# Kernel tuning notes

Hardware: AMD Instinct MI355X
Metric: run time of the kernel (lower is better)

The kernel has to match this reference:

```python
import jax, jax.numpy as jnp
import numpy as np

N = 128      # numNodes
F_IN = 128   # numFeatures
H = 64       # numHiddens
C = 40       # numClasses
K = 2        # numLayers (SGConv hops)
B = 4096     # batch
NTRIL = N * (N + 1) // 2


def setup_inputs() -> dict:
    key = jax.random.key(0)
    ks = jax.random.split(key, 6)
    x = jax.random.normal(ks[0], (B, N, F_IN), dtype=jnp.float32)
    edge_w = jax.random.uniform(ks[1], (NTRIL,), dtype=jnp.float32)  # learnable tril edge weights (positive init)
    lin_w = jax.random.normal(ks[2], (F_IN, H), dtype=jnp.float32) / np.float32(np.sqrt(F_IN))
    lin_b = jnp.zeros((H,), dtype=jnp.float32)
    conv_w = jax.random.normal(ks[3], (N,), dtype=jnp.float32) / np.float32(np.sqrt(N))  # Conv1d(N,1,1) weight
    conv_b = jnp.zeros((1,), dtype=jnp.float32)
    fc_w = jax.random.normal(ks[4], (H, C), dtype=jnp.float32) / np.float32(np.sqrt(H))
    fc_b = jnp.zeros((C,), dtype=jnp.float32)
    return {"x": x, "edge_w": edge_w, "lin_w": lin_w, "lin_b": lin_b,
            "conv_w": conv_w, "conv_b": conv_b, "fc_w": fc_w, "fc_b": fc_b}


def reference(x, edge_w, lin_w, lin_b, conv_w, conv_b, fc_w, fc_b):
    # Rebuild symmetric dense adjacency from tril-parameterized edge weights
    xs, ys = jnp.tril_indices(N)
    A = jnp.zeros((N, N), dtype=jnp.float32).at[xs, ys].set(edge_w)
    A = A + A.T - jnp.diag(jnp.diag(A))                 # symmetrize (keep diag once)
    A_hat = A + jnp.eye(N, dtype=jnp.float32)           # add_self_loops(fill_value=1)
    # SGConv symmetric normalization: D^-1/2 (A+I) D^-1/2
    deg = A_hat.sum(axis=1)
    dinv = jnp.where(deg > 0, deg ** -0.5, 0.0)
    A_norm = dinv[:, None] * A_hat * dinv[None, :]
    # K-hop propagation over node dim (memory-bound stream of [B,N,F])
    h = x
    for _ in range(K):
        h = jnp.einsum('ij,bjf->bif', A_norm, h)
    h = jax.nn.relu(h @ lin_w + lin_b)                  # SGConv linear + relu -> [B,N,H]
    pooled = jnp.einsum('bnh,n->bh', h, conv_w) + conv_b  # Conv1d(N->1, kernel=1) over nodes
    pooled = jax.nn.relu(pooled)
    return pooled @ fc_w + fc_b                         # [B, C]
```

## Files before the change

kernel.cpp:

```cpp
#include <hip/hip_runtime.h>
#include <math.h>

#define N     128
#define F_INN 128
#define HD    64
#define NC    40
#define BB    4096

#define CHUNK     16
#define XS_STRIDE 17
#define YS_STRIDE 68

__global__ void prep_anorm(const float* __restrict__ edge_w,
                           float* __restrict__ An_out) {
    __shared__ float Ah[N][N + 1];
    __shared__ float dinv[N];
    const int t  = threadIdx.x;
    const int i  = t >> 1;
    const int jh = (t & 1) * 64;
    for (int jj = 0; jj < 64; ++jj) {
        int j  = jh + jj;
        int hi = i >= j ? i : j;
        int lo = i >= j ? j : i;
        float a = edge_w[hi * (hi + 1) / 2 + lo];
        if (i == j) a += 1.0f;
        Ah[i][j] = a;
    }
    __syncthreads();
    if (t < N) {
        float s = 0.0f;
        for (int j = 0; j < N; ++j) s += Ah[t][j];
        dinv[t] = s > 0.0f ? 1.0f / sqrtf(s) : 0.0f;
    }
    __syncthreads();
    for (int jj = 0; jj < 64; ++jj) {
        int j = jh + jj;
        An_out[i * N + j] = dinv[i] * Ah[i][j] * dinv[j];
    }
}

__global__ void prep_a2(const float* __restrict__ An, float* __restrict__ A2) {
    const int i = blockIdx.x;
    const int j = threadIdx.x;
    float acc = 0.0f;
    for (int k = 0; k < N; ++k)
        acc += An[i * N + k] * An[k * N + j];
    A2[i * N + j] = acc;
}

__global__ __launch_bounds__(256, 2) void dgcnn_main(
    const float* __restrict__ x, const float* __restrict__ A2,
    const float* __restrict__ lin_w, const float* __restrict__ lin_b,
    const float* __restrict__ conv_w, const float* __restrict__ conv_b,
    const float* __restrict__ fc_w, const float* __restrict__ fc_b,
    float* __restrict__ out) {
    __shared__ float lw[F_INN * HD];
    __shared__ float ys[N * YS_STRIDE];
    __shared__ float xs[N * XS_STRIDE];
    __shared__ float pooled[HD];

    const int t  = threadIdx.x;
    const int b  = blockIdx.x;
    const int tm = t & 31;
    const int hg = t >> 5;
    const int h0 = hg * 8;

    {
        const float4* g = (const float4*)lin_w;
        float4* s = (float4*)lw;
#pragma unroll
        for (int r = 0; r < 8; ++r) s[t + 256 * r] = g[t + 256 * r];
    }

    float acc[4][8];
#pragma unroll
    for (int r = 0; r < 4; ++r)
#pragma unroll
        for (int q = 0; q < 8; ++q) acc[r][q] = 0.0f;

    const float* xb = x + (size_t)b * (N * F_INN);

    for (int f0 = 0; f0 < F_INN; f0 += CHUNK) {
        __syncthreads();
        {
            const float4* g = (const float4*)xb;
#pragma unroll
            for (int r = 0; r < 2; ++r) {
                int l4 = t + 256 * r;
                int n  = l4 >> 2;
                int fq = l4 & 3;
                float4 v = g[n * 32 + (f0 >> 2) + fq];
                float* d = &xs[n * XS_STRIDE + fq * 4];
                d[0] = v.x; d[1] = v.y; d[2] = v.z; d[3] = v.w;
            }
        }
        __syncthreads();
#pragma unroll
        for (int f = 0; f < CHUNK; ++f) {
            float av[4];
#pragma unroll
            for (int r = 0; r < 4; ++r) av[r] = xs[(tm + 32 * r) * XS_STRIDE + f];
            const float4* lr = (const float4*)&lw[(f0 + f) * HD];
            float4 w0 = lr[hg * 2];
            float4 w1 = lr[hg * 2 + 1];
            float wv[8] = {w0.x, w0.y, w0.z, w0.w, w1.x, w1.y, w1.z, w1.w};
#pragma unroll
            for (int r = 0; r < 4; ++r)
#pragma unroll
                for (int q = 0; q < 8; ++q)
                    acc[r][q] = fmaf(av[r], wv[q], acc[r][q]);
        }
    }

#pragma unroll
    for (int r = 0; r < 4; ++r) {
        int n = tm + 32 * r;
#pragma unroll
        for (int q = 0; q < 8; ++q) {
            ys[n * YS_STRIDE + h0 + q] = acc[r][q];
            acc[r][q] = 0.0f;
        }
    }

    for (int j0 = 0; j0 < N; j0 += CHUNK) {
        __syncthreads();
        {
            const float4* g = (const float4*)A2;
#pragma unroll
            for (int r = 0; r < 2; ++r) {
                int l4 = t + 256 * r;
                int n  = l4 >> 2;
                int jq = l4 & 3;
                float4 v = g[n * 32 + (j0 >> 2) + jq];
                float* d = &xs[n * XS_STRIDE + jq * 4];
                d[0] = v.x; d[1] = v.y; d[2] = v.z; d[3] = v.w;
            }
        }
        __syncthreads();
#pragma unroll
        for (int j = 0; j < CHUNK; ++j) {
            float av[4];
#pragma unroll
            for (int r = 0; r < 4; ++r) av[r] = xs[(tm + 32 * r) * XS_STRIDE + j];
            const float4* yr = (const float4*)&ys[(j0 + j) * YS_STRIDE];
            float4 w0 = yr[hg * 2];
            float4 w1 = yr[hg * 2 + 1];
            float wv[8] = {w0.x, w0.y, w0.z, w0.w, w1.x, w1.y, w1.z, w1.w};
#pragma unroll
            for (int r = 0; r < 4; ++r)
#pragma unroll
                for (int q = 0; q < 8; ++q)
                    acc[r][q] = fmaf(av[r], wv[q], acc[r][q]);
        }
    }

    __syncthreads();

#pragma unroll
    for (int r = 0; r < 4; ++r) {
        int n = tm + 32 * r;
        float cw = conv_w[n];
#pragma unroll
        for (int q = 0; q < 8; ++q) {
            float v = acc[r][q] + lin_b[h0 + q];
            v = fmaxf(v, 0.0f);
            ys[n * YS_STRIDE + h0 + q] = v * cw;
        }
    }
    __syncthreads();

    if (t < HD) {
        float s = 0.0f;
        for (int n = 0; n < N; ++n) s += ys[n * YS_STRIDE + t];
        pooled[t] = fmaxf(s + conv_b[0], 0.0f);
    }
    __syncthreads();

    if (t < NC) {
        float o = fc_b[t];
        for (int h = 0; h < HD; ++h) o += pooled[h] * fc_w[h * NC + t];
        out[(size_t)b * NC + t] = o;
    }
}

extern "C" void kernel_launch(void* const* d_in, const int* in_sizes, int n_in,
                              void* d_out, int out_size, void* d_ws, size_t ws_size,
                              hipStream_t stream) {
    const float* x      = (const float*)d_in[0];
    const float* edge_w = (const float*)d_in[1];
    const float* lin_w  = (const float*)d_in[2];
    const float* lin_b  = (const float*)d_in[3];
    const float* conv_w = (const float*)d_in[4];
    const float* conv_b = (const float*)d_in[5];
    const float* fc_w   = (const float*)d_in[6];
    const float* fc_b   = (const float*)d_in[7];
    float* out = (float*)d_out;

    float* A2 = (float*)d_ws;
    float* An = A2 + N * N;

    prep_anorm<<<1, 256, 0, stream>>>(edge_w, An);
    prep_a2<<<N, N, 0, stream>>>(An, A2);
    dgcnn_main<<<BB, 256, 0, stream>>>(x, A2, lin_w, lin_b, conv_w, conv_b,
                                       fc_w, fc_b, out);
}
```

Before: 602.0 us.

## Double-buffer transposed x/A2 tiles and alias LDS to raise occupancy

Rewrites the main kernel's tile staging to use a transposed, double-buffered shared tile with register prefetch of the next chunk, so global loads overlap the FMA loop and each thread reads contiguous float4 node values. The lin_w and intermediate ys buffers now share one LDS allocation, which reduces shared memory per block, and launch bounds are raised to three blocks per CU. The node pooling reduction is also split across all threads. The cost is more register pressure under the tighter launch bound and bank conflicts from the transposed scatter stores.

Measured after the change: 1.186 ms. 1.97x slower.

```diff
diff --git a/kernel.cpp b/kernel.cpp
--- a/kernel.cpp
+++ b/kernel.cpp
@@ -2,14 +2,10 @@
 #include <math.h>
 
 #define N     128
-#define F_INN 128
-#define HD    64
 #define NC    40
 #define BB    4096
-
-#define CHUNK     16
-#define XS_STRIDE 17
-#define YS_STRIDE 68
+#define XT_S  132
+#define YS_S  68
 
 __global__ void prep_anorm(const float* __restrict__ edge_w,
                            float* __restrict__ An_out) {
@@ -48,22 +44,25 @@
     A2[i * N + j] = acc;
 }
 
-__global__ __launch_bounds__(256, 2) void dgcnn_main(
+__global__ __launch_bounds__(256, 3) void dgcnn_main(
     const float* __restrict__ x, const float* __restrict__ A2,
     const float* __restrict__ lin_w, const float* __restrict__ lin_b,
     const float* __restrict__ conv_w, const float* __restrict__ conv_b,
     const float* __restrict__ fc_w, const float* __restrict__ fc_b,
     float* __restrict__ out) {
-    __shared__ float lw[F_INN * HD];
-    __shared__ float ys[N * YS_STRIDE];
-    __shared__ float xs[N * XS_STRIDE];
-    __shared__ float pooled[HD];
+    __shared__ __align__(16) float uni[N * YS_S];
+    __shared__ __align__(16) float xs[2][16 * XT_S];
+    float* lw = uni;
+    float* ys = uni;
 
     const int t  = threadIdx.x;
     const int b  = blockIdx.x;
     const int tm = t & 31;
     const int hg = t >> 5;
     const int h0 = hg * 8;
+    const int n0 = 4 * tm;
+
+    const float* xb = x + (size_t)b * (N * N);
 
     {
         const float4* g = (const float4*)lin_w;
@@ -71,6 +70,20 @@
 #pragma unroll
         for (int r = 0; r < 8; ++r) s[t + 256 * r] = g[t + 256 * r];
     }
+    {
+        const float4* g = (const float4*)xb;
+#pragma unroll
+        for (int half = 0; half < 2; ++half) {
+            int l4 = t + 256 * half;
+            int n = l4 >> 2, fq = l4 & 3;
+            float4 v = g[n * 32 + fq];
+            float* d = &xs[0][0];
+            d[(4 * fq + 0) * XT_S + n] = v.x;
+            d[(4 * fq + 1) * XT_S + n] = v.y;
+            d[(4 * fq + 2) * XT_S + n] = v.z;
+            d[(4 * fq + 3) * XT_S + n] = v.w;
+        }
+    }
 
     float acc[4][8];
 #pragma unroll
@@ -78,107 +91,140 @@
 #pragma unroll
         for (int q = 0; q < 8; ++q) acc[r][q] = 0.0f;
 
-    const float* xb = x + (size_t)b * (N * F_INN);
-
-    for (int f0 = 0; f0 < F_INN; f0 += CHUNK) {
+    __syncthreads();
+
+#pragma unroll 1
+    for (int c = 0; c < 8; ++c) {
+        float4 pf[2];
+        int pn[2], pq[2];
+        {
+            const float4* g = (c == 7) ? (const float4*)A2 : (const float4*)xb;
+            const int f0q = (c == 7) ? 0 : (c + 1) * 4;
+#pragma unroll
+            for (int half = 0; half < 2; ++half) {
+                int l4 = t + 256 * half;
+                pn[half] = l4 >> 2; pq[half] = l4 & 3;
+                pf[half] = g[pn[half] * 32 + f0q + pq[half]];
+            }
+        }
+        const float* xsb = &xs[c & 1][0];
+        const int fb = c * 16;
+#pragma unroll
+        for (int f = 0; f < 16; ++f) {
+            float4 av = *(const float4*)&xsb[f * XT_S + n0];
+            float4 w0 = *(const float4*)&lw[(fb + f) * 64 + h0];
+            float4 w1 = *(const float4*)&lw[(fb + f) * 64 + h0 + 4];
+            float a[4] = {av.x, av.y, av.z, av.w};
+            float w[8] = {w0.x, w0.y, w0.z, w0.w, w1.x, w1.y, w1.z, w1.w};
+#pragma unroll
+            for (int r = 0; r < 4; ++r)
+#pragma unroll
+                for (int q = 0; q < 8; ++q)
+                    acc[r][q] = fmaf(a[r], w[q], acc[r][q]);
+        }
+        {
+            float* d = &xs[(c + 1) & 1][0];
+#pragma unroll
+            for (int half = 0; half < 2; ++half) {
+                d[(4 * pq[half] + 0) * XT_S + pn[half]] = pf[half].x;
+                d[(4 * pq[half] + 1) * XT_S + pn[half]] = pf[half].y;
+                d[(4 * pq[half] + 2) * XT_S + pn[half]] = pf[half].z;
+                d[(4 * pq[half] + 3) * XT_S + pn[half]] = pf[half].w;
+            }
+        }
         __syncthreads();
-        {
-            const float4* g = (const float4*)xb;
-#pragma unroll
-            for (int r = 0; r < 2; ++r) {
-                int l4 = t + 256 * r;
-                int n  = l4 >> 2;
-                int fq = l4 & 3;
-                float4 v = g[n * 32 + (f0 >> 2) + fq];
-                float* d = &xs[n * XS_STRIDE + fq * 4];
-                d[0] = v.x; d[1] = v.y; d[2] = v.z; d[3] = v.w;
+    }
+
+#pragma unroll
+    for (int r = 0; r < 4; ++r) {
+        float4 a0 = make_float4(acc[r][0], acc[r][1], acc[r][2], acc[r][3]);
+        float4 a1 = make_float4(acc[r][4], acc[r][5], acc[r][6], acc[r][7]);
+        *(float4*)&ys[(n0 + r) * YS_S + h0] = a0;
+        *(float4*)&ys[(n0 + r) * YS_S + h0 + 4] = a1;
+#pragma unroll
+        for (int q = 0; q < 8; ++q) acc[r][q] = 0.0f;
+    }
+    __syncthreads();
+
+#pragma unroll 1
+    for (int c = 0; c < 8; ++c) {
+        float4 pf[2];
+        int pn[2], pq[2];
+        if (c < 7) {
+            const float4* g = (const float4*)A2;
+            const int f0q = (c + 1) * 4;
+#pragma unroll
+            for (int half = 0; half < 2; ++half) {
+                int l4 = t + 256 * half;
+                pn[half] = l4 >> 2; pq[half] = l4 & 3;
+                pf[half] = g[pn[half] * 32 + f0q + pq[half]];
+            }
+        }
+        const float* xsb = &xs[c & 1][0];
+        const int jb = c * 16;
+#pragma unroll
+        for (int j = 0; j < 16; ++j) {
+            float4 av = *(const float4*)&xsb[j * XT_S + n0];
+            float4 w0 = *(const float4*)&ys[(jb + j) * YS_S + h0];
+            float4 w1 = *(const float4*)&ys[(jb + j) * YS_S + h0 + 4];
+            float a[4] = {av.x, av.y, av.z, av.w};
+            float w[8] = {w0.x, w0.y, w0.z, w0.w, w1.x, w1.y, w1.z, w1.w};
+#pragma unroll
+            for (int r = 0; r < 4; ++r)
+#pragma unroll
+                for (int q = 0; q < 8; ++q)
+                    acc[r][q] = fmaf(a[r], w[q], acc[r][q]);
+        }
+        if (c < 7) {
+            float* d = &xs[(c + 1) & 1][0];
+#pragma unroll
+            for (int half = 0; half < 2; ++half) {
+                d[(4 * pq[half] + 0) * XT_S + pn[half]] = pf[half].x;
+                d[(4 * pq[half] + 1) * XT_S + pn[half]] = pf[half].y;
+                d[(4 * pq[half] + 2) * XT_S + pn[half]] = pf[half].z;
+                d[(4 * pq[half] + 3) * XT_S + pn[half]] = pf[half].w;
             }
         }
         __syncthreads();
-#pragma unroll
-        for (int f = 0; f < CHUNK; ++f) {
-            float av[4];
-#pragma unroll
-            for (int r = 0; r < 4; ++r) av[r] = xs[(tm + 32 * r) * XS_STRIDE + f];
-            const float4* lr = (const float4*)&lw[(f0 + f) * HD];
-            float4 w0 = lr[hg * 2];
-            float4 w1 = lr[hg * 2 + 1];
-            float wv[8] = {w0.x, w0.y, w0.z, w0.w, w1.x, w1.y, w1.z, w1.w};
-#pragma unroll
-            for (int r = 0; r < 4; ++r)
-#pragma unroll
-                for (int q = 0; q < 8; ++q)
-                    acc[r][q] = fmaf(av[r], wv[q], acc[r][q]);
-        }
     }
 
 #pragma unroll
     for (int r = 0; r < 4; ++r) {
-        int n = tm + 32 * r;
-#pragma unroll
-        for (int q = 0; q < 8; ++q) {
-            ys[n * YS_STRIDE + h0 + q] = acc[r][q];
-            acc[r][q] = 0.0f;
-        }
-    }
-
-    for (int j0 = 0; j0 < N; j0 += CHUNK) {
-        __syncthreads();
-        {
-            const float4* g = (const float4*)A2;
-#pragma unroll
-            for (int r = 0; r < 2; ++r) {
-                int l4 = t + 256 * r;
-                int n  = l4 >> 2;
-                int jq = l4 & 3;
-                float4 v = g[n * 32 + (j0 >> 2) + jq];
-                float* d = &xs[n * XS_STRIDE + jq * 4];
-                d[0] = v.x; d[1] = v.y; d[2] = v.z; d[3] = v.w;
-            }
-        }
-        __syncthreads();
-#pragma unroll
-        for (int j = 0; j < CHUNK; ++j) {
-            float av[4];
-#pragma unroll
-            for (int r = 0; r < 4; ++r) av[r] = xs[(tm + 32 * r) * XS_STRIDE + j];
-            const float4* yr = (const float4*)&ys[(j0 + j) * YS_STRIDE];
-            float4 w0 = yr[hg * 2];
-            float4 w1 = yr[hg * 2 + 1];
-            float wv[8] = {w0.x, w0.y, w0.z, w0.w, w1.x, w1.y, w1.z, w1.w};
-#pragma unroll
-            for (int r = 0; r < 4; ++r)
-#pragma unroll
-                for (int q = 0; q < 8; ++q)
-                    acc[r][q] = fmaf(av[r], wv[q], acc[r][q]);
-        }
-    }
-
-    __syncthreads();
-
-#pragma unroll
-    for (int r = 0; r < 4; ++r) {
-        int n = tm + 32 * r;
+        int n = n0 + r;
         float cw = conv_w[n];
-#pragma unroll
-        for (int q = 0; q < 8; ++q) {
-            float v = acc[r][q] + lin_b[h0 + q];
-            v = fmaxf(v, 0.0f);
-            ys[n * YS_STRIDE + h0 + q] = v * cw;
-        }
-    }
-    __syncthreads();
-
-    if (t < HD) {
+        float4 v0, v1;
+        v0.x = fmaxf(acc[r][0] + lin_b[h0 + 0], 0.0f) * cw;
+        v0.y = fmaxf(acc[r][1] + lin_b[h0 + 1], 0.0f) * cw;
+        v0.z = fmaxf(acc[r][2] + lin_b[h0 + 2], 0.0f) * cw;
+        v0.w = fmaxf(acc[r][3] + lin_b[h0 + 3], 0.0f) * cw;
+        v1.x = fmaxf(acc[r][4] + lin_b[h0 + 4], 0.0f) * cw;
+        v1.y = fmaxf(acc[r][5] + lin_b[h0 + 5], 0.0f) * cw;
+        v1.z = fmaxf(acc[r][6] + lin_b[h0 + 6], 0.0f) * cw;
+        v1.w = fmaxf(acc[r][7] + lin_b[h0 + 7], 0.0f) * cw;
+        *(float4*)&ys[n * YS_S + h0] = v0;
+        *(float4*)&ys[n * YS_S + h0 + 4] = v1;
+    }
+    __syncthreads();
+
+    float* ps   = &xs[0][0];
+    float* pool = &xs[1][0];
+    {
+        int h = t & 63, qr = t >> 6;
         float s = 0.0f;
-        for (int n = 0; n < N; ++n) s += ys[n * YS_STRIDE + t];
-        pooled[t] = fmaxf(s + conv_b[0], 0.0f);
-    }
-    __syncthreads();
-
+#pragma unroll
+        for (int i = 0; i < 32; ++i) s += ys[(qr * 32 + i) * YS_S + h];
+        ps[qr * 64 + h] = s;
+    }
+    __syncthreads();
+    if (t < 64) {
+        float s = ps[t] + ps[64 + t] + ps[128 + t] + ps[192 + t] + conv_b[0];
+        pool[t] = fmaxf(s, 0.0f);
+    }
+    __syncthreads();
     if (t < NC) {
         float o = fc_b[t];
-        for (int h = 0; h < HD; ++h) o += pooled[h] * fc_w[h * NC + t];
+#pragma unroll
+        for (int h = 0; h < 64; ++h) o += pool[h] * fc_w[h * NC + t];
         out[(size_t)b * NC + t] = o;
     }
 }
```
